# Optimization experiments

Measured on AMD Instinct MI355X. Metric: run time of the kernel, lower is better.

The kernel has to match this reference:

```python
import jax, jax.numpy as jnp
import numpy as np

B, T, N, E, H, L, K = 2, 32, 256, 1024, 16, 2, 256
MAXLEN = 512  # RelativeMultiheadAttention max_seq_len default
SCALES = (1, 2, 4)
TAU = 1.0


def setup_inputs() -> dict:
    key = jax.random.key(0)
    ks = jax.random.split(key, 9)
    s = 0.02
    A = 2 * L  # [layer0-spatial, layer0-temporal, layer1-spatial, layer1-temporal]
    return {
        "x": jax.random.normal(ks[0], (B, T, N, E), jnp.float32),
        "attn_wq": jax.random.normal(ks[1], (A, E, E), jnp.float32) * s,
        "attn_bq": jnp.zeros((A, E), jnp.float32),
        "attn_wk": jax.random.normal(ks[2], (A, E, E), jnp.float32) * s,
        "attn_bk": jnp.zeros((A, E), jnp.float32),
        "attn_wv": jax.random.normal(ks[3], (A, E, E), jnp.float32) * s,
        "attn_bv": jnp.zeros((A, E), jnp.float32),
        "attn_wd": jax.random.normal(ks[4], (A, E, E), jnp.float32) * s,
        "attn_bd": jnp.zeros((A, E), jnp.float32),
        "rel_bias": jax.random.normal(ks[5], (A, 2 * MAXLEN - 1, H), jnp.float32) * s,
        "sel_w": jax.random.normal(ks[6], (E, K), jnp.float32) * s,
        "sel_b": jnp.zeros((K,), jnp.float32),
    }


def _rel_attn(x, wq, bq, wk, bk, wv, bv, wd, bd, rb):
    # x: [Bx, S, E]; rb: [2*MAXLEN-1, H]
    Bx, S, _ = x.shape
    D = E // H
    q = (x @ wq + bq).reshape(Bx, S, H, D)
    k = (x @ wk + bk).reshape(Bx, S, H, D)
    v = (x @ wv + bv).reshape(Bx, S, H, D)
    scores = jnp.einsum('bshd,bthd->bhst', q, k) / jnp.sqrt(jnp.asarray(D, x.dtype))
    pos = jnp.arange(S)
    idx = pos[None, :] - pos[:, None] + (MAXLEN - 1)  # [S, S]
    bias = rb[idx]  # [S, S, H] gathered relative-position bias
    scores = scores + bias.transpose(2, 0, 1)[None]
    w = jax.nn.softmax(scores, axis=-1)
    ctx = jnp.einsum('bhst,bthd->bshd', w, v).reshape(Bx, S, E)
    return ctx @ wd + bd


def reference(x, attn_wq, attn_bq, attn_wk, attn_bk, attn_wv, attn_bv,
              attn_wd, attn_bd, rel_bias, sel_w, sel_b):
    h = x
    for l in range(L):
        # spatial attention over tokens within each frame
        i = 2 * l
        hs = h.reshape(B * T, N, E)
        hs = _rel_attn(hs, attn_wq[i], attn_bq[i], attn_wk[i], attn_bk[i],
                       attn_wv[i], attn_bv[i], attn_wd[i], attn_bd[i], rel_bias[i])
        # temporal attention across frames per spatial location
        j = 2 * l + 1
        ht = hs.reshape(B, T, N, E).transpose(0, 2, 1, 3).reshape(B * N, T, E)
        ht = _rel_attn(ht, attn_wq[j], attn_bq[j], attn_wk[j], attn_bk[j],
                       attn_wv[j], attn_bv[j], attn_wd[j], attn_bd[j], rel_bias[j])
        h = ht.reshape(B, N, T, E).transpose(0, 2, 1, 3)
    # DifferentiableTokenSelection: softmax-weighted pooling into K tokens
    flat = h.reshape(B, T * N, E)
    sc = flat @ sel_w + sel_b  # [B, T*N, K]
    wts = jax.nn.softmax(sc / TAU, axis=1)
    sel = jnp.einsum('bmk,bme->bke', wts, flat)  # [B, K, E]
    # multi-scale average pooling (kernel==stride==scale), concat along tokens
    outs = [sel.reshape(B, K // s, s, E).mean(axis=2) for s in SCALES]
    return jnp.concatenate(outs, axis=1)  # [B, K + K//2 + K//4, E]
```

## Files before the change

### kernel.cpp

```cpp
#include <hip/hip_runtime.h>
#include <stdint.h>


using f16x8 = __attribute__((ext_vector_type(8))) _Float16;
using f16x4 = __attribute__((ext_vector_type(4))) _Float16;
using f32x4 = __attribute__((ext_vector_type(4))) float;

__device__ __forceinline__ int tmap_dev(int m) {
    int bx = m >> 5;
    int s  = m & 31;
    int b  = bx >> 8;
    int n  = bx & 255;
    return (((b << 5) + s) << 8) + n;
}

__device__ __forceinline__ void load16(const _Float16* g, _Float16* l)
{
    __builtin_amdgcn_global_load_lds(
        (const __attribute__((address_space(1))) unsigned int*)g,
        (__attribute__((address_space(3))) unsigned int*)l,
        16, 0, 0);
}

__device__ __forceinline__ void split_f16(float v, _Float16& h, _Float16& l)
{
    h = (_Float16)v;
    l = (_Float16)(v - (float)h);
}

__global__ __launch_bounds__(256)
void conv_act(const float* __restrict__ src, _Float16* __restrict__ dh,
              _Float16* __restrict__ dl, int m_off)
{
    int idx = blockIdx.x * 256 + threadIdx.x;
    int e = idx << 3;
    int ml = e >> 10, col = e & 1023;
    const float* s = src + (size_t)(m_off + ml) * 1024 + col;
    float4 a = *(const float4*)s;
    float4 b = *(const float4*)(s + 4);
    float vv[8] = {a.x, a.y, a.z, a.w, b.x, b.y, b.z, b.w};
    f16x8 vh, vl;
    #pragma unroll
    for (int r = 0; r < 8; r++) {
        _Float16 h, l;
        split_f16(vv[r], h, l);
        vh[r] = h; vl[r] = l;
    }
    *(f16x8*)(dh + (size_t)ml * 1024 + col) = vh;
    *(f16x8*)(dl + (size_t)ml * 1024 + col) = vl;
}

__global__ __launch_bounds__(256)
void conv_wT(const float* __restrict__ W, _Float16* __restrict__ Th,
             _Float16* __restrict__ Tl, int ncols)
{
    __shared__ float Ls[64][65];
    const int n0 = blockIdx.x * 64, k0 = blockIdx.y * 64;
    const int t = threadIdx.x;
    const int kk = t >> 4, nn = (t & 15) << 2;
    #pragma unroll
    for (int i = 0; i < 4; i++) {
        float4 v = *(const float4*)(W + (size_t)(k0 + kk + 16 * i) * ncols + n0 + nn);
        Ls[kk + 16 * i][nn + 0] = v.x; Ls[kk + 16 * i][nn + 1] = v.y;
        Ls[kk + 16 * i][nn + 2] = v.z; Ls[kk + 16 * i][nn + 3] = v.w;
    }
    __syncthreads();
    const int nl = t >> 4, kc = (t & 15) << 2;
    #pragma unroll
    for (int i = 0; i < 4; i++) {
        int n = nl + 16 * i;
        f16x4 hh, ll;
        #pragma unroll
        for (int c = 0; c < 4; c++) {
            _Float16 h, l;
            split_f16(Ls[kc + c][n], h, l);
            hh[c] = h; ll[c] = l;
        }
        *(f16x4*)(Th + (size_t)(n0 + n) * 1024 + k0 + kc) = hh;
        *(f16x4*)(Tl + (size_t)(n0 + n) * 1024 + k0 + kc) = ll;
    }
}

template<int EPI>
__device__ __forceinline__ void gemm_core(
    const _Float16* __restrict__ Ah, const _Float16* __restrict__ Al,
    const _Float16* __restrict__ Wh, const _Float16* __restrict__ Wl,
    const float* __restrict__ bias,
    float* __restrict__ C, _Float16* __restrict__ Ch, _Float16* __restrict__ Cl,
    int ldc, int map_in, int m_off_in, int map_out, int m_off_out,
    int n0, int m0)
{
    __shared__ uint32_t smem_u[8512];
    _Float16* smem = (_Float16*)smem_u;
    _Float16* sAh = smem;
    _Float16* sAl = smem + 4096;
    _Float16* sBh = smem + 8192;
    _Float16* sBl = smem + 12288;

    const int tid = threadIdx.x;
    const int lane = tid & 63;
    const int wv = tid >> 6;
    const int fm = (wv >> 1) << 6;
    const int fn = (wv & 1) << 6;
    const int lm = lane & 15, lq = lane >> 4;

    f32x4 acc[4][4] = {};

    const int srow = tid >> 2;
    const int skc  = (tid & 3) << 3;
    const int gm0 = m_off_in + m0 + srow;
    const int gm1 = gm0 + 64;
    const int r0 = map_in ? tmap_dev(gm0) : gm0;
    const int r1 = map_in ? tmap_dev(gm1) : gm1;
    const _Float16* gAh0 = Ah + (size_t)r0 * 1024 + skc;
    const _Float16* gAh1 = Ah + (size_t)r1 * 1024 + skc;
    const _Float16* gAl0 = Al + (size_t)r0 * 1024 + skc;
    const _Float16* gAl1 = Al + (size_t)r1 * 1024 + skc;
    const _Float16* gB0 = Wh + (size_t)(n0 + srow) * 1024 + skc;
    const _Float16* gB1 = Wl + (size_t)(n0 + srow) * 1024 + skc;
    const int lo = tid << 3;

    for (int k0 = 0; k0 < 1024; k0 += 32) {
        load16(gAh0 + k0, sAh + lo);
        load16(gAh1 + k0, sAh + lo + 2048);
        load16(gAl0 + k0, sAl + lo);
        load16(gAl1 + k0, sAl + lo + 2048);
        load16(gB0 + k0,         sBh + lo);
        load16(gB0 + k0 + 65536, sBh + lo + 2048);
        load16(gB1 + k0,         sBl + lo);
        load16(gB1 + k0 + 65536, sBl + lo + 2048);
        __syncthreads();

        f16x8 ah[4], al[4], bh[4], bl[4];
        #pragma unroll
        for (int i = 0; i < 4; i++) {
            int ra = (fm + i * 16 + lm) * 32 + lq * 8;
            ah[i] = *(const f16x8*)(sAh + ra);
            al[i] = *(const f16x8*)(sAl + ra);
            int rb_ = (fn + i * 16 + lm) * 32 + lq * 8;
            bh[i] = *(const f16x8*)(sBh + rb_);
            bl[i] = *(const f16x8*)(sBl + rb_);
        }
        #pragma unroll
        for (int i = 0; i < 4; i++)
            #pragma unroll
            for (int j = 0; j < 4; j++) {
                acc[i][j] = __builtin_amdgcn_mfma_f32_16x16x32_f16(ah[i], bh[j], acc[i][j], 0, 0, 0);
                acc[i][j] = __builtin_amdgcn_mfma_f32_16x16x32_f16(ah[i], bl[j], acc[i][j], 0, 0, 0);
                acc[i][j] = __builtin_amdgcn_mfma_f32_16x16x32_f16(al[i], bh[j], acc[i][j], 0, 0, 0);
            }
        __syncthreads();
    }

    if (EPI == 0 || EPI == 1) {
        #pragma unroll
        for (int j = 0; j < 4; j++) {
            int n = n0 + fn + j * 16 + lm;
            float bb = bias[n];
            #pragma unroll
            for (int i = 0; i < 4; i++) {
                #pragma unroll
                for (int r = 0; r < 4; r++) {
                    int gm = m_off_out + m0 + fm + i * 16 + lq * 4 + r;
                    int row = map_out ? tmap_dev(gm) : gm;
                    float v = acc[i][j][r] + bb;
                    if (EPI == 0) {
                        C[(size_t)row * ldc + n] = v;
                    } else {
                        _Float16 h, l;
                        split_f16(v, h, l);
                        Ch[(size_t)row * 1024 + n] = h;
                        Cl[(size_t)row * 1024 + n] = l;
                    }
                }
            }
        }
    } else {
        const int fmh = fm >> 6;
        #pragma unroll
        for (int mh = 0; mh < 2; mh++) {
            __syncthreads();
            if (fmh == mh) {
                #pragma unroll
                for (int j = 0; j < 4; j++) {
                    int n = fn + j * 16 + lm;
                    float bb = bias[n0 + n];
                    #pragma unroll
                    for (int i = 0; i < 4; i++) {
                        #pragma unroll
                        for (int r = 0; r < 4; r++) {
                            float v = acc[i][j][r] + bb;
                            _Float16 h, l;
                            split_f16(v, h, l);
                            uint32_t ph = (uint32_t)__builtin_bit_cast(unsigned short, h);
                            uint32_t pl = (uint32_t)__builtin_bit_cast(unsigned short, l);
                            smem_u[(i * 16 + lq * 4 + r) * 133 + n] = ph | (pl << 16);
                        }
                    }
                }
            }
            __syncthreads();
            #pragma unroll
            for (int g = 0; g < 8; g++) {
                int u = tid + g * 256;
                int nn = u >> 4;
                int mg = (u & 15) << 2;
                uint32_t p0 = smem_u[(mg + 0) * 133 + nn];
                uint32_t p1 = smem_u[(mg + 1) * 133 + nn];
                uint32_t p2 = smem_u[(mg + 2) * 133 + nn];
                uint32_t p3 = smem_u[(mg + 3) * 133 + nn];
                f16x4 hh, ll;
                hh[0] = __builtin_bit_cast(_Float16, (unsigned short)(p0 & 0xffff));
                hh[1] = __builtin_bit_cast(_Float16, (unsigned short)(p1 & 0xffff));
                hh[2] = __builtin_bit_cast(_Float16, (unsigned short)(p2 & 0xffff));
                hh[3] = __builtin_bit_cast(_Float16, (unsigned short)(p3 & 0xffff));
                ll[0] = __builtin_bit_cast(_Float16, (unsigned short)(p0 >> 16));
                ll[1] = __builtin_bit_cast(_Float16, (unsigned short)(p1 >> 16));
                ll[2] = __builtin_bit_cast(_Float16, (unsigned short)(p2 >> 16));
                ll[3] = __builtin_bit_cast(_Float16, (unsigned short)(p3 >> 16));
                size_t off = (size_t)(n0 + nn) * 8192 + (m0 + mh * 64 + mg);
                *(f16x4*)(Ch + off) = hh;
                *(f16x4*)(Cl + off) = ll;
            }
        }
    }
}

__global__ __launch_bounds__(256, 2)
void gemm_f16s_f32(const _Float16* __restrict__ Ah, const _Float16* __restrict__ Al,
                   int map_in, int m_off_in,
                   const _Float16* __restrict__ Wh, const _Float16* __restrict__ Wl,
                   const float* __restrict__ bias, float* __restrict__ C, int ldc,
                   int map_out, int m_off_out)
{
    gemm_core<0>(Ah, Al, Wh, Wl, bias, C, nullptr, nullptr, ldc,
                 map_in, m_off_in, map_out, m_off_out,
                 blockIdx.x * 128, blockIdx.y * 128);
}

template<int EPI>
__device__ __forceinline__ void gemm256_core(
    uint32_t* __restrict__ smem_u,
    const _Float16* __restrict__ Ah, const _Float16* __restrict__ Al,
    const _Float16* __restrict__ Wh, const _Float16* __restrict__ Wl,
    const float* __restrict__ bias,
    _Float16* __restrict__ Ch, _Float16* __restrict__ Cl,
    int map_in, int m_off_in, int map_out, int m_off_out,
    int n0, int m0)
{
    _Float16* S = (_Float16*)smem_u;
    const int tid  = threadIdx.x;
    const int lane = tid & 63;
    const int wv = tid >> 6;
    const int wm = wv >> 1;
    const int fm = wm << 6;
    const int fn = (wv & 1) << 6;
    const int lm = lane & 15, lq = lane >> 4;
    const int ko = ((lq ^ ((lm >> 1) & 3)) << 3);

    f32x4 acc[4][4] = {};

    const int srow = tid >> 2;
    const int scol = (((tid & 3) ^ ((tid >> 3) & 3)) << 3);
    const int gm0 = m_off_in + m0 + srow;
    const int gm1 = gm0 + 128;
    const int r0 = map_in ? tmap_dev(gm0) : gm0;
    const int r1 = map_in ? tmap_dev(gm1) : gm1;
    const _Float16* gAh0 = Ah + (size_t)r0 * 1024 + scol;
    const _Float16* gAh1 = Ah + (size_t)r1 * 1024 + scol;
    const _Float16* gAl0 = Al + (size_t)r0 * 1024 + scol;
    const _Float16* gAl1 = Al + (size_t)r1 * 1024 + scol;
    const _Float16* gBh  = Wh + (size_t)(n0 + srow) * 1024 + scol;
    const _Float16* gBl  = Wl + (size_t)(n0 + srow) * 1024 + scol;
    const int lo = tid << 3;

    auto stage = [&](int t, int b) {
        const int k0 = t << 5;
        _Float16* d = S + b * 24576;
        load16(gAh0 + k0, d + lo);
        load16(gAh1 + k0, d + 4096  + lo);
        load16(gAl0 + k0, d + 8192  + lo);
        load16(gAl1 + k0, d + 12288 + lo);
        load16(gBh  + k0, d + 16384 + lo);
        load16(gBl  + k0, d + 20480 + lo);
    };

    auto kstep = [&](int t, int cb, int sb, bool last) {
        if (last) asm volatile("s_waitcnt vmcnt(0) lgkmcnt(0)" ::: "memory");
        else      asm volatile("s_waitcnt vmcnt(6) lgkmcnt(0)" ::: "memory");
        __builtin_amdgcn_s_barrier();
        if (sb >= 0) stage(t + 2, sb);

        const _Float16* c = S + cb * 24576;
        f16x8 ah[4], al[4], bh[4], bl[4];
        #pragma unroll
        for (int i = 0; i < 4; i++) {
            int ra = (fm + i * 16 + lm) * 32 + ko;
            ah[i] = *(const f16x8*)(c + ra);
            al[i] = *(const f16x8*)(c + 8192 + ra);
            int rb = (fn + i * 16 + lm) * 32 + ko;
            bh[i] = *(const f16x8*)(c + 16384 + rb);
            bl[i] = *(const f16x8*)(c + 20480 + rb);
        }
        __builtin_amdgcn_s_setprio(1);
        #pragma unroll
        for (int i = 0; i < 4; i++)
            #pragma unroll
            for (int j = 0; j < 4; j++) {
                acc[i][j] = __builtin_amdgcn_mfma_f32_16x16x32_f16(ah[i], bh[j], acc[i][j], 0, 0, 0);
                acc[i][j] = __builtin_amdgcn_mfma_f32_16x16x32_f16(ah[i], bl[j], acc[i][j], 0, 0, 0);
                acc[i][j] = __builtin_amdgcn_mfma_f32_16x16x32_f16(al[i], bh[j], acc[i][j], 0, 0, 0);
            }
        __builtin_amdgcn_s_setprio(0);
    };

    stage(0, 0);
    stage(1, 1);
    #pragma unroll 1
    for (int tt = 0; tt < 30; tt += 3) {
        kstep(tt + 0, 0, 2, false);
        kstep(tt + 1, 1, 0, false);
        kstep(tt + 2, 2, 1, false);
    }
    kstep(30, 0, -1, false);
    kstep(31, 1, -1, true);

    if (EPI == 1) {
        #pragma unroll
        for (int j = 0; j < 4; j++) {
            int n = n0 + fn + j * 16 + lm;
            float bb = bias[n];
            #pragma unroll
            for (int i = 0; i < 4; i++) {
                #pragma unroll
                for (int r = 0; r < 4; r++) {
                    int gm = m_off_out + m0 + fm + i * 16 + lq * 4 + r;
                    int row = map_out ? tmap_dev(gm) : gm;
                    float v = acc[i][j][r] + bb;
                    _Float16 h, l;
                    split_f16(v, h, l);
                    Ch[(size_t)row * 1024 + n] = h;
                    Cl[(size_t)row * 1024 + n] = l;
                }
            }
        }
    } else {
        #pragma unroll 1
        for (int q = 0; q < 4; q++) {
            __syncthreads();
            if (wm == q) {
                #pragma unroll
                for (int j = 0; j < 4; j++) {
                    int ncol = fn + j * 16 + lm;
                    float bb = bias[n0 + ncol];
                    #pragma unroll
                    for (int i = 0; i < 4; i++) {
                        #pragma unroll
                        for (int r = 0; r < 4; r++) {
                            float v = acc[i][j][r] + bb;
                            _Float16 h, l;
                            split_f16(v, h, l);
                            uint32_t ph = (uint32_t)__builtin_bit_cast(unsigned short, h);
                            uint32_t pl = (uint32_t)__builtin_bit_cast(unsigned short, l);
                            smem_u[(i * 16 + lq * 4 + r) * 129 + ncol] = ph | (pl << 16);
                        }
                    }
                }
            }
            __syncthreads();
            #pragma unroll
            for (int g = 0; g < 4; g++) {
                int u = tid + g * 512;
                int nn = u >> 4;
                int mg = (u & 15) << 2;
                uint32_t p0 = smem_u[(mg + 0) * 129 + nn];
                uint32_t p1 = smem_u[(mg + 1) * 129 + nn];
                uint32_t p2 = smem_u[(mg + 2) * 129 + nn];
                uint32_t p3 = smem_u[(mg + 3) * 129 + nn];
                f16x4 hh, ll;
                hh[0] = __builtin_bit_cast(_Float16, (unsigned short)(p0 & 0xffff));
                hh[1] = __builtin_bit_cast(_Float16, (unsigned short)(p1 & 0xffff));
                hh[2] = __builtin_bit_cast(_Float16, (unsigned short)(p2 & 0xffff));
                hh[3] = __builtin_bit_cast(_Float16, (unsigned short)(p3 & 0xffff));
                ll[0] = __builtin_bit_cast(_Float16, (unsigned short)(p0 >> 16));
                ll[1] = __builtin_bit_cast(_Float16, (unsigned short)(p1 >> 16));
                ll[2] = __builtin_bit_cast(_Float16, (unsigned short)(p2 >> 16));
                ll[3] = __builtin_bit_cast(_Float16, (unsigned short)(p3 >> 16));
                size_t off = (size_t)(n0 + nn) * 8192 + (m0 + q * 64 + mg);
                *(f16x4*)(Ch + off) = hh;
                *(f16x4*)(Cl + off) = ll;
            }
        }
    }
}

__global__ __launch_bounds__(512, 2)
void gemm_qkv256(const _Float16* __restrict__ Ah, const _Float16* __restrict__ Al,
                 int map_in, int m_off_in,
                 const _Float16* __restrict__ WTh, const _Float16* __restrict__ WTl,
                 const float* __restrict__ bq, const float* __restrict__ bk,
                 const float* __restrict__ bv,
                 _Float16* __restrict__ Qh, _Float16* __restrict__ Ql,
                 _Float16* __restrict__ Kh, _Float16* __restrict__ Kl,
                 _Float16* __restrict__ VTh, _Float16* __restrict__ VTl)
{
    __shared__ uint32_t smem_u[36864];
    const int bid = blockIdx.x;
    const int wg = (bid & 7) * 96 + (bid >> 3);
    const int z = wg >> 8;
    const int rem = wg & 255;
    const int m0 = (rem >> 3) << 8;
    const int n0 = (rem & 7) << 7;
    const _Float16* wh = WTh + (size_t)z * 1048576;
    const _Float16* wl = WTl + (size_t)z * 1048576;
    if (z < 2) {
        const float* bb = (z == 0) ? bq : bk;
        _Float16* oh = (z == 0) ? Qh : Kh;
        _Float16* ol = (z == 0) ? Ql : Kl;
        gemm256_core<1>(smem_u, Ah, Al, wh, wl, bb, oh, ol,
                        map_in, m_off_in, 0, 0, n0, m0);
    } else {
        gemm256_core<3>(smem_u, Ah, Al, wh, wl, bv, VTh, VTl,
                        map_in, m_off_in, 0, 0, n0, m0);
    }
}

__global__ __launch_bounds__(512, 2)
void gemm_h256(const _Float16* __restrict__ Ah, const _Float16* __restrict__ Al,
               int map_in, int m_off_in,
               const _Float16* __restrict__ Wh, const _Float16* __restrict__ Wl,
               const float* __restrict__ bias,
               _Float16* __restrict__ Ch, _Float16* __restrict__ Cl,
               int map_out, int m_off_out)
{
    __shared__ uint32_t smem_u[36864];
    const int bid = blockIdx.x;
    const int wg = (bid & 7) * 32 + (bid >> 3);
    const int m0 = (wg >> 3) << 8;
    const int n0 = (wg & 7) << 7;
    gemm256_core<1>(smem_u, Ah, Al, Wh, Wl, bias, Ch, Cl,
                    map_in, m_off_in, map_out, m_off_out, n0, m0);
}

__global__ __launch_bounds__(256, 2)
void attn_s_m(const _Float16* __restrict__ Qh, const _Float16* __restrict__ Ql,
              const _Float16* __restrict__ Kh, const _Float16* __restrict__ Kl,
              const _Float16* __restrict__ VTh, const _Float16* __restrict__ VTl,
              const float* __restrict__ RB,
              _Float16* __restrict__ Ch, _Float16* __restrict__ Cl)
{
    __shared__ _Float16 sKh[2048], sKl[2048];
    __shared__ _Float16 sVh[2560], sVl[2560];
    __shared__ _Float16 sPh[4][2560], sPl[4][2560];
    __shared__ float Bt[512];

    const int tid = threadIdx.x;
    const int lane = tid & 63;
    const int w = tid >> 6;
    const int lm = lane & 15, lq = lane >> 4;
    const int frame = blockIdx.x;
    const int h = blockIdx.y;
    const int rowbase = frame * 256;

    #pragma unroll
    for (int l = 0; l < 2; l++) {
        int idx = tid + l * 256;
        if (idx < 511) Bt[idx] = RB[(size_t)(256 + idx) * 16 + h];
    }

    f16x8 qbh[4][2], qbl[4][2];
    #pragma unroll
    for (int st = 0; st < 4; st++)
        #pragma unroll
        for (int kk = 0; kk < 2; kk++) {
            size_t qo = (size_t)(rowbase + w * 64 + st * 16 + lm) * 1024
                        + h * 64 + kk * 32 + lq * 8;
            qbh[st][kk] = *(const f16x8*)(Qh + qo);
            qbl[st][kk] = *(const f16x8*)(Ql + qo);
        }

    f32x4 cacc[4][4] = {};
    float lsum[4] = {0.f, 0.f, 0.f, 0.f};
    _Float16* Ph = sPh[w];
    _Float16* Pl = sPl[w];

    const int skrow = tid >> 3, skd = (tid & 7) << 3;
    const int svrow = tid >> 2, svj = (tid & 3) << 3;

    for (int jc = 0; jc < 8; jc++) {
        __syncthreads();
        {
            size_t ko = (size_t)(rowbase + jc * 32 + skrow) * 1024 + h * 64 + skd;
            *(f16x8*)(sKh + skrow * 64 + skd) = *(const f16x8*)(Kh + ko);
            *(f16x8*)(sKl + skrow * 64 + skd) = *(const f16x8*)(Kl + ko);
            size_t vo = (size_t)(h * 64 + svrow) * 8192 + rowbase + jc * 32 + svj;
            *(f16x8*)(sVh + svrow * 40 + svj) = *(const f16x8*)(VTh + vo);
            *(f16x8*)(sVl + svrow * 40 + svj) = *(const f16x8*)(VTl + vo);
        }
        __syncthreads();

        f32x4 sacc[2][4] = {};
        #pragma unroll
        for (int jt = 0; jt < 2; jt++) {
            f16x8 kah[2], kal[2];
            #pragma unroll
            for (int kk = 0; kk < 2; kk++) {
                int ra = (jt * 16 + lm) * 64 + kk * 32 + lq * 8;
                kah[kk] = *(const f16x8*)(sKh + ra);
                kal[kk] = *(const f16x8*)(sKl + ra);
            }
            #pragma unroll
            for (int st = 0; st < 4; st++)
                #pragma unroll
                for (int kk = 0; kk < 2; kk++) {
                    sacc[jt][st] = __builtin_amdgcn_mfma_f32_16x16x32_f16(kah[kk], qbh[st][kk], sacc[jt][st], 0, 0, 0);
                    sacc[jt][st] = __builtin_amdgcn_mfma_f32_16x16x32_f16(kah[kk], qbl[st][kk], sacc[jt][st], 0, 0, 0);
                    sacc[jt][st] = __builtin_amdgcn_mfma_f32_16x16x32_f16(kal[kk], qbh[st][kk], sacc[jt][st], 0, 0, 0);
                }
        }

        #pragma unroll
        for (int jt = 0; jt < 2; jt++)
            #pragma unroll
            for (int st = 0; st < 4; st++) {
                f16x4 p4h, p4l;
                #pragma unroll
                for (int r = 0; r < 4; r++) {
                    int j = jc * 32 + jt * 16 + lq * 4 + r;
                    int s = w * 64 + st * 16 + lm;
                    float p = __expf(sacc[jt][st][r] * 0.125f + Bt[j - s + 255]);
                    lsum[st] += p;
                    _Float16 hp, lp;
                    split_f16(p, hp, lp);
                    p4h[r] = hp; p4l[r] = lp;
                }
                int pa = (st * 16 + lm) * 40 + jt * 16 + lq * 4;
                *(f16x4*)(Ph + pa) = p4h;
                *(f16x4*)(Pl + pa) = p4l;
            }

        #pragma unroll
        for (int st = 0; st < 4; st++) {
            int pb = (st * 16 + lm) * 40 + lq * 8;
            f16x8 pbh = *(const f16x8*)(Ph + pb);
            f16x8 pbl = *(const f16x8*)(Pl + pb);
            #pragma unroll
            for (int dt = 0; dt < 4; dt++) {
                int va = (dt * 16 + lm) * 40 + lq * 8;
                f16x8 vah = *(const f16x8*)(sVh + va);
                f16x8 val = *(const f16x8*)(sVl + va);
                cacc[dt][st] = __builtin_amdgcn_mfma_f32_16x16x32_f16(vah, pbh, cacc[dt][st], 0, 0, 0);
                cacc[dt][st] = __builtin_amdgcn_mfma_f32_16x16x32_f16(vah, pbl, cacc[dt][st], 0, 0, 0);
                cacc[dt][st] = __builtin_amdgcn_mfma_f32_16x16x32_f16(val, pbh, cacc[dt][st], 0, 0, 0);
            }
        }
    }

    float inv[4];
    #pragma unroll
    for (int st = 0; st < 4; st++) {
        float t = lsum[st];
        t += __shfl_xor(t, 16);
        t += __shfl_xor(t, 32);
        inv[st] = 1.0f / t;
    }

    #pragma unroll
    for (int st = 0; st < 4; st++)
        #pragma unroll
        for (int dt = 0; dt < 4; dt++) {
            f16x4 oh, ol;
            #pragma unroll
            for (int r = 0; r < 4; r++) {
                _Float16 hp, lp;
                split_f16(cacc[dt][st][r] * inv[st], hp, lp);
                oh[r] = hp; ol[r] = lp;
            }
            size_t oo = (size_t)(rowbase + w * 64 + st * 16 + lm) * 1024
                        + h * 64 + dt * 16 + lq * 4;
            *(f16x4*)(Ch + oo) = oh;
            *(f16x4*)(Cl + oo) = ol;
        }
}

__global__ __launch_bounds__(256, 2)
void attn_t_m(const _Float16* __restrict__ Qh, const _Float16* __restrict__ Ql,
              const _Float16* __restrict__ Kh, const _Float16* __restrict__ Kl,
              const _Float16* __restrict__ VTh, const _Float16* __restrict__ VTl,
              const float* __restrict__ RB,
              _Float16* __restrict__ Ch, _Float16* __restrict__ Cl)
{
    __shared__ _Float16 sPh[4][1280], sPl[4][1280];
    __shared__ float Bt[64];

    const int tid = threadIdx.x;
    const int lane = tid & 63;
    const int w = tid >> 6;
    const int lm = lane & 15, lq = lane >> 4;
    const int h = blockIdx.y;
    const int bx = blockIdx.x * 4 + w;
    const int rowbase = bx * 32;

    if (tid < 63) Bt[tid] = RB[(size_t)(480 + tid) * 16 + h];
    __syncthreads();

    f16x8 qbh[2][2], qbl[2][2];
    #pragma unroll
    for (int st = 0; st < 2; st++)
        #pragma unroll
        for (int kk = 0; kk < 2; kk++) {
            size_t qo = (size_t)(rowbase + st * 16 + lm) * 1024 + h * 64 + kk * 32 + lq * 8;
            qbh[st][kk] = *(const f16x8*)(Qh + qo);
            qbl[st][kk] = *(const f16x8*)(Ql + qo);
        }

    f32x4 sacc[2][2] = {};
    #pragma unroll
    for (int jt = 0; jt < 2; jt++) {
        f16x8 kah[2], kal[2];
        #pragma unroll
        for (int kk = 0; kk < 2; kk++) {
            size_t ko = (size_t)(rowbase + jt * 16 + lm) * 1024 + h * 64 + kk * 32 + lq * 8;
            kah[kk] = *(const f16x8*)(Kh + ko);
            kal[kk] = *(const f16x8*)(Kl + ko);
        }
        #pragma unroll
        for (int st = 0; st < 2; st++)
            #pragma unroll
            for (int kk = 0; kk < 2; kk++) {
                sacc[jt][st] = __builtin_amdgcn_mfma_f32_16x16x32_f16(kah[kk], qbh[st][kk], sacc[jt][st], 0, 0, 0);
                sacc[jt][st] = __builtin_amdgcn_mfma_f32_16x16x32_f16(kah[kk], qbl[st][kk], sacc[jt][st], 0, 0, 0);
                sacc[jt][st] = __builtin_amdgcn_mfma_f32_16x16x32_f16(kal[kk], qbh[st][kk], sacc[jt][st], 0, 0, 0);
            }
    }

    float lsum[2] = {0.f, 0.f};
    _Float16* Ph = sPh[w];
    _Float16* Pl = sPl[w];
    #pragma unroll
    for (int jt = 0; jt < 2; jt++)
        #pragma unroll
        for (int st = 0; st < 2; st++) {
            f16x4 p4h, p4l;
            #pragma unroll
            for (int r = 0; r < 4; r++) {
                int j = jt * 16 + lq * 4 + r;
                int s = st * 16 + lm;
                float p = __expf(sacc[jt][st][r] * 0.125f + Bt[j - s + 31]);
                lsum[st] += p;
                _Float16 hp, lp;
                split_f16(p, hp, lp);
                p4h[r] = hp; p4l[r] = lp;
            }
            int pa = (st * 16 + lm) * 40 + jt * 16 + lq * 4;
            *(f16x4*)(Ph + pa) = p4h;
            *(f16x4*)(Pl + pa) = p4l;
        }

    f16x8 vah[4], val[4];
    #pragma unroll
    for (int dt = 0; dt < 4; dt++) {
        size_t vo = (size_t)(h * 64 + dt * 16 + lm) * 8192 + rowbase + lq * 8;
        vah[dt] = *(const f16x8*)(VTh + vo);
        val[dt] = *(const f16x8*)(VTl + vo);
    }
    f32x4 cacc[4][2] = {};
    #pragma unroll
    for (int st = 0; st < 2; st++) {
        int pb = (st * 16 + lm) * 40 + lq * 8;
        f16x8 pbh = *(const f16x8*)(Ph + pb);
        f16x8 pbl = *(const f16x8*)(Pl + pb);
        #pragma unroll
        for (int dt = 0; dt < 4; dt++) {
            cacc[dt][st] = __builtin_amdgcn_mfma_f32_16x16x32_f16(vah[dt], pbh, cacc[dt][st], 0, 0, 0);
            cacc[dt][st] = __builtin_amdgcn_mfma_f32_16x16x32_f16(vah[dt], pbl, cacc[dt][st], 0, 0, 0);
            cacc[dt][st] = __builtin_amdgcn_mfma_f32_16x16x32_f16(val[dt], pbh, cacc[dt][st], 0, 0, 0);
        }
    }

    float inv[2];
    #pragma unroll
    for (int st = 0; st < 2; st++) {
        float t = lsum[st];
        t += __shfl_xor(t, 16);
        t += __shfl_xor(t, 32);
        inv[st] = 1.0f / t;
    }

    #pragma unroll
    for (int st = 0; st < 2; st++)
        #pragma unroll
        for (int dt = 0; dt < 4; dt++) {
            f16x4 oh, ol;
            #pragma unroll
            for (int r = 0; r < 4; r++) {
                _Float16 hp, lp;
                split_f16(cacc[dt][st][r] * inv[st], hp, lp);
                oh[r] = hp; ol[r] = lp;
            }
            size_t oo = (size_t)(rowbase + st * 16 + lm) * 1024 + h * 64 + dt * 16 + lq * 4;
            *(f16x4*)(Ch + oo) = oh;
            *(f16x4*)(Cl + oo) = ol;
        }
}

__global__ __launch_bounds__(256)
void colsum_part_kernel(const float* __restrict__ SC, float* __restrict__ P)
{
    int bid = blockIdx.x;
    int b = bid >> 7, chunk = bid & 127;
    int base = b * 8192 + chunk * 64;
    int k = threadIdx.x;
    float sum = 0.0f;
    for (int r = 0; r < 64; r++)
        sum += __expf(SC[(size_t)(base + r) * 256 + k]);
    P[(size_t)bid * 256 + k] = sum;
}

__global__ __launch_bounds__(256)
void colsum_reduce_kernel(const float* __restrict__ P, float* __restrict__ CS)
{
    int b = blockIdx.x;
    int k = threadIdx.x;
    float s = 0.0f;
    for (int c = 0; c < 128; c++)
        s += P[(size_t)(b * 128 + c) * 256 + k];
    CS[b * 256 + k] = s;
}

__global__ __launch_bounds__(256)
void trans_wts(const float* __restrict__ SC, const float* __restrict__ CS,
               _Float16* __restrict__ Th, _Float16* __restrict__ Tl)
{
    __shared__ float L[64][65];
    const int mt = blockIdx.x * 64;
    const int kt = blockIdx.y * 64;
    const int b  = mt >> 13;
    const int ml = mt & 8191;
    const int tid = threadIdx.x;
    #pragma unroll
    for (int l = 0; l < 4; l++) {
        int idx = tid + 256 * l;
        int r = idx >> 4, c4 = (idx & 15) << 2;
        float4 v = *(const float4*)(SC + (size_t)(mt + r) * 256 + kt + c4);
        L[r][c4 + 0] = __expf(v.x); L[r][c4 + 1] = __expf(v.y);
        L[r][c4 + 2] = __expf(v.z); L[r][c4 + 3] = __expf(v.w);
    }
    __syncthreads();
    #pragma unroll
    for (int l = 0; l < 4; l++) {
        int idx = tid + 256 * l;
        int rk = idx >> 4, c4 = (idx & 15) << 2;
        float inv = 1.0f / CS[b * 256 + kt + rk];
        f16x4 hh, ll;
        #pragma unroll
        for (int u = 0; u < 4; u++) {
            _Float16 h, l2;
            split_f16(L[c4 + u][rk] * inv, h, l2);
            hh[u] = h; ll[u] = l2;
        }
        size_t o = ((size_t)b * 256 + kt + rk) * 8192 + ml + c4;
        *(f16x4*)(Th + o) = hh;
        *(f16x4*)(Tl + o) = ll;
    }
}

__global__ __launch_bounds__(256)
void trans_f16(const _Float16* __restrict__ Sh, const _Float16* __restrict__ Sl,
               _Float16* __restrict__ Th, _Float16* __restrict__ Tl)
{
    __shared__ _Float16 L[64][72];
    const int mt = blockIdx.x * 64, et = blockIdx.y * 64;
    const _Float16* S = blockIdx.z ? Sl : Sh;
    _Float16* T = blockIdx.z ? Tl : Th;
    const int tid = threadIdx.x;
    #pragma unroll
    for (int l = 0; l < 2; l++) {
        int v = tid * 2 + l;
        int r = v >> 3, c8 = (v & 7) << 3;
        *(f16x8*)&L[r][c8] = *(const f16x8*)(S + (size_t)(mt + r) * 1024 + et + c8);
    }
    __syncthreads();
    #pragma unroll
    for (int l = 0; l < 2; l++) {
        int v = tid * 2 + l;
        int r = v >> 3, c8 = (v & 7) << 3;
        f16x8 o;
        #pragma unroll
        for (int u = 0; u < 8; u++) o[u] = L[c8 + u][r];
        *(f16x8*)(T + (size_t)(et + r) * 16384 + mt + c8) = o;
    }
}

__global__ __launch_bounds__(256, 2)
void gemm_selm(const _Float16* __restrict__ Wth, const _Float16* __restrict__ Wtl,
               const _Float16* __restrict__ Hth, const _Float16* __restrict__ Htl,
               float* __restrict__ P)
{
    __shared__ _Float16 sAh[4096], sAl[4096], sBh[4096], sBl[4096];
    const int tid = threadIdx.x;
    const int lane = tid & 63;
    const int wv = tid >> 6;
    const int fm = (wv >> 1) << 6;
    const int fn = (wv & 1) << 6;
    const int lm = lane & 15, lq = lane >> 4;
    const int n0 = blockIdx.x * 128;
    const int m0 = blockIdx.y * 128;
    const int z  = blockIdx.z;
    const int b = z >> 3, sp = z & 7;

    f32x4 acc[4][4] = {};

    const int srow = tid >> 2;
    const int skc  = (tid & 3) << 3;
    const _Float16* gAh0 = Wth + ((size_t)b * 256 + m0 + srow) * 8192 + sp * 1024 + skc;
    const _Float16* gAl0 = Wtl + ((size_t)b * 256 + m0 + srow) * 8192 + sp * 1024 + skc;
    const _Float16* gB0 = Hth + (size_t)(n0 + srow) * 16384 + b * 8192 + sp * 1024 + skc;
    const _Float16* gB1 = Htl + (size_t)(n0 + srow) * 16384 + b * 8192 + sp * 1024 + skc;
    const int lo = tid << 3;

    for (int k0 = 0; k0 < 1024; k0 += 32) {
        load16(gAh0 + k0,          sAh + lo);
        load16(gAh0 + k0 + 524288, sAh + lo + 2048);
        load16(gAl0 + k0,          sAl + lo);
        load16(gAl0 + k0 + 524288, sAl + lo + 2048);
        load16(gB0 + k0,           sBh + lo);
        load16(gB0 + k0 + 1048576, sBh + lo + 2048);
        load16(gB1 + k0,           sBl + lo);
        load16(gB1 + k0 + 1048576, sBl + lo + 2048);
        __syncthreads();

        f16x8 ah[4], al[4], bh[4], bl[4];
        #pragma unroll
        for (int i = 0; i < 4; i++) {
            int ra = (fm + i * 16 + lm) * 32 + lq * 8;
            ah[i] = *(const f16x8*)(sAh + ra);
            al[i] = *(const f16x8*)(sAl + ra);
            int rb_ = (fn + i * 16 + lm) * 32 + lq * 8;
            bh[i] = *(const f16x8*)(sBh + rb_);
            bl[i] = *(const f16x8*)(sBl + rb_);
        }
        #pragma unroll
        for (int i = 0; i < 4; i++)
            #pragma unroll
            for (int j = 0; j < 4; j++) {
                acc[i][j] = __builtin_amdgcn_mfma_f32_16x16x32_f16(ah[i], bh[j], acc[i][j], 0, 0, 0);
                acc[i][j] = __builtin_amdgcn_mfma_f32_16x16x32_f16(ah[i], bl[j], acc[i][j], 0, 0, 0);
                acc[i][j] = __builtin_amdgcn_mfma_f32_16x16x32_f16(al[i], bh[j], acc[i][j], 0, 0, 0);
            }
        __syncthreads();
    }

    float* Pz = P + (size_t)z * 262144;
    #pragma unroll
    for (int j = 0; j < 4; j++) {
        int n = n0 + fn + j * 16 + lm;
        #pragma unroll
        for (int i = 0; i < 4; i++)
            #pragma unroll
            for (int r = 0; r < 4; r++) {
                int k = m0 + fm + i * 16 + lq * 4 + r;
                Pz[(size_t)k * 1024 + n] = acc[i][j][r];
            }
    }
}

__global__ __launch_bounds__(256)
void sel_reduce(const float* __restrict__ P, float* __restrict__ SEL)
{
    int idx4 = blockIdx.x * 256 + threadIdx.x;
    int e = idx4 << 2;
    int b = e >> 18;
    int rest = e & 262143;
    const float* p = P + (size_t)(b * 8) * 262144 + rest;
    float4 acc = {0.f, 0.f, 0.f, 0.f};
    #pragma unroll
    for (int s = 0; s < 8; s++) {
        float4 v = *(const float4*)(p + (size_t)s * 262144);
        acc.x += v.x; acc.y += v.y; acc.z += v.z; acc.w += v.w;
    }
    *(float4*)(SEL + e) = acc;
}

__global__ __launch_bounds__(256)
void pool_kernel(const float* __restrict__ SEL, float* __restrict__ out)
{
    int i4 = blockIdx.x * 256 + threadIdx.x;
    int e  = i4 << 2;
    int row = e >> 10;
    int b = row / 448;
    int r = row - b * 448;
    int c = e & 1023;
    const float* sb = SEL + (size_t)b * (256 * 1024);
    float4 o;
    if (r < 256) {
        o = *(const float4*)(sb + (size_t)r * 1024 + c);
    } else if (r < 384) {
        int r2 = (r - 256) * 2;
        float4 x0 = *(const float4*)(sb + (size_t)r2 * 1024 + c);
        float4 x1 = *(const float4*)(sb + (size_t)(r2 + 1) * 1024 + c);
        o.x = 0.5f * (x0.x + x1.x); o.y = 0.5f * (x0.y + x1.y);
        o.z = 0.5f * (x0.z + x1.z); o.w = 0.5f * (x0.w + x1.w);
    } else {
        int r4 = (r - 384) * 4;
        float4 x0 = *(const float4*)(sb + (size_t)(r4 + 0) * 1024 + c);
        float4 x1 = *(const float4*)(sb + (size_t)(r4 + 1) * 1024 + c);
        float4 x2 = *(const float4*)(sb + (size_t)(r4 + 2) * 1024 + c);
        float4 x3 = *(const float4*)(sb + (size_t)(r4 + 3) * 1024 + c);
        o.x = 0.25f * (x0.x + x1.x + x2.x + x3.x);
        o.y = 0.25f * (x0.y + x1.y + x2.y + x3.y);
        o.z = 0.25f * (x0.z + x1.z + x2.z + x3.z);
        o.w = 0.25f * (x0.w + x1.w + x2.w + x3.w);
    }
    *(float4*)(out + e) = o;
}

extern "C" void kernel_launch(void* const* d_in, const int* in_sizes, int n_in,
                              void* d_out, int out_size, void* d_ws, size_t ws_size,
                              hipStream_t stream)
{
    const float* x    = (const float*)d_in[0];
    const float* wq   = (const float*)d_in[1];
    const float* bq   = (const float*)d_in[2];
    const float* wk   = (const float*)d_in[3];
    const float* bk   = (const float*)d_in[4];
    const float* wv   = (const float*)d_in[5];
    const float* bv   = (const float*)d_in[6];
    const float* wd   = (const float*)d_in[7];
    const float* bd   = (const float*)d_in[8];
    const float* rb   = (const float*)d_in[9];
    const float* selw = (const float*)d_in[10];
    const float* selb = (const float*)d_in[11];
    float* out = (float*)d_out;

    float* base = (float*)d_ws;
    _Float16* Hh  = (_Float16*)base;
    _Float16* Hl  = Hh + 16777216;
    _Float16* Qh  = (_Float16*)(base + 16777216);
    _Float16* Ql  = Qh + 8388608;
    _Float16* Kh  = Ql + 8388608;
    _Float16* Kl  = Kh + 8388608;
    _Float16* VTh = (_Float16*)(base + 33554432);
    _Float16* VTl = VTh + 8388608;
    _Float16* CXh = (_Float16*)(base + 41943040);
    _Float16* CXl = CXh + 8388608;
    _Float16* WTh = (_Float16*)(base + 50331648);
    _Float16* WTl = WTh + 4194304;
    _Float16* Ah  = (_Float16*)(base + 54525952);
    _Float16* Al  = Ah + 8388608;
    float* SC   = (float*)Qh;
    float* Pp   = (float*)Kh;
    float* SEL  = (float*)Kl;
    float* PART = SEL + 524288;
    float* CSUM = PART + 65536;
    _Float16* WTTh = CXh;
    _Float16* WTTl = CXl;
    _Float16* HTh  = Ah;
    _Float16* HTl  = VTh;

    const dim3 blk(256);
    const dim3 blk2(512);

    for (int a = 0; a < 4; a++) {
        const int mi = (a & 1);
        const size_t wo = (size_t)a * 1048576;
        const int bo = a * 1024;
        const float* rba = rb + (size_t)a * 1023 * 16;

        conv_wT<<<dim3(16, 16), blk, 0, stream>>>(wq + wo, WTh,           WTl,           1024);
        conv_wT<<<dim3(16, 16), blk, 0, stream>>>(wk + wo, WTh + 1048576, WTl + 1048576, 1024);
        conv_wT<<<dim3(16, 16), blk, 0, stream>>>(wv + wo, WTh + 2097152, WTl + 2097152, 1024);
        conv_wT<<<dim3(16, 16), blk, 0, stream>>>(wd + wo, WTh + 3145728, WTl + 3145728, 1024);

        for (int c = 0; c < 2; c++) {
            const int mo = c * 8192;
            const _Float16 *sH, *sL;
            int sm, so;
            if (a == 0) {
                conv_act<<<4096, blk, 0, stream>>>(x, Ah, Al, mo);
                sH = Ah; sL = Al; sm = 0; so = 0;
            } else {
                sH = Hh; sL = Hl; sm = mi; so = mo;
            }
            gemm_qkv256<<<dim3(768), blk2, 0, stream>>>(
                sH, sL, sm, so, WTh, WTl, bq + bo, bk + bo, bv + bo,
                Qh, Ql, Kh, Kl, VTh, VTl);
            if (mi == 0)
                attn_s_m<<<dim3(32, 16), blk, 0, stream>>>(Qh, Ql, Kh, Kl, VTh, VTl, rba, CXh, CXl);
            else
                attn_t_m<<<dim3(64, 16), blk, 0, stream>>>(Qh, Ql, Kh, Kl, VTh, VTl, rba, CXh, CXl);
            gemm_h256<<<dim3(256), blk2, 0, stream>>>(
                CXh, CXl, 0, 0, WTh + 3145728, WTl + 3145728, bd + bo, Hh, Hl, mi, mo);
        }
    }

    conv_wT<<<dim3(4, 16), blk, 0, stream>>>(selw, WTh, WTl, 256);
    gemm_f16s_f32<<<dim3(2, 128), blk, 0, stream>>>(
        Hh, Hl, 0, 0, WTh, WTl, selb, SC, 256, 0, 0);
    colsum_part_kernel<<<256, blk, 0, stream>>>(SC, PART);
    colsum_reduce_kernel<<<2, blk, 0, stream>>>(PART, CSUM);
    trans_wts<<<dim3(256, 4), blk, 0, stream>>>(SC, CSUM, WTTh, WTTl);
    trans_f16<<<dim3(256, 16, 2), blk, 0, stream>>>(Hh, Hl, HTh, HTl);
    gemm_selm<<<dim3(8, 2, 16), blk, 0, stream>>>(WTTh, WTTl, HTh, HTl, Pp);
    sel_reduce<<<512, blk, 0, stream>>>(Pp, SEL);
    pool_kernel<<<896, blk, 0, stream>>>(SEL, out);
}
```

Before: 2.124 ms.

## Interleave GEMM mainloop into barrier-separated phases and stage EPI1 stores via LDS

Splits each k-step of the 256-row GEMM into four phases, one per B column fragment. Each phase issues a part of the next tile's global-to-LDS loads, then runs MFMAs between explicit barriers and sched_barriers, aiming at a finer interleave of memory and matrix work across waves. The EPI==1 epilogue for this kernel now goes through LDS and writes 16-byte vector stores of the hi/lo halves instead of scattered 2-byte stores. The dead EPI1/EPI2 paths in the older gemm_core are removed. The extra barriers per k-step add synchronisation cost and could hurt if waves stall.

```diff
diff --git a/kernel.cpp b/kernel.cpp
--- a/kernel.cpp
+++ b/kernel.cpp
@@ -152,7 +152,7 @@
         __syncthreads();
     }
 
-    if (EPI == 0 || EPI == 1) {
+    if (EPI == 0) {
         #pragma unroll
         for (int j = 0; j < 4; j++) {
             int n = n0 + fn + j * 16 + lm;
@@ -163,64 +163,8 @@
                 for (int r = 0; r < 4; r++) {
                     int gm = m_off_out + m0 + fm + i * 16 + lq * 4 + r;
                     int row = map_out ? tmap_dev(gm) : gm;
-                    float v = acc[i][j][r] + bb;
-                    if (EPI == 0) {
-                        C[(size_t)row * ldc + n] = v;
-                    } else {
-                        _Float16 h, l;
-                        split_f16(v, h, l);
-                        Ch[(size_t)row * 1024 + n] = h;
-                        Cl[(size_t)row * 1024 + n] = l;
-                    }
+                    C[(size_t)row * ldc + n] = acc[i][j][r] + bb;
                 }
-            }
-        }
-    } else {
-        const int fmh = fm >> 6;
-        #pragma unroll
-        for (int mh = 0; mh < 2; mh++) {
-            __syncthreads();
-            if (fmh == mh) {
-                #pragma unroll
-                for (int j = 0; j < 4; j++) {
-                    int n = fn + j * 16 + lm;
-                    float bb = bias[n0 + n];
-                    #pragma unroll
-                    for (int i = 0; i < 4; i++) {
-                        #pragma unroll
-                        for (int r = 0; r < 4; r++) {
-                            float v = acc[i][j][r] + bb;
-                            _Float16 h, l;
-                            split_f16(v, h, l);
-                            uint32_t ph = (uint32_t)__builtin_bit_cast(unsigned short, h);
-                            uint32_t pl = (uint32_t)__builtin_bit_cast(unsigned short, l);
-                            smem_u[(i * 16 + lq * 4 + r) * 133 + n] = ph | (pl << 16);
-                        }
-                    }
-                }
-            }
-            __syncthreads();
-            #pragma unroll
-            for (int g = 0; g < 8; g++) {
-                int u = tid + g * 256;
-                int nn = u >> 4;
-                int mg = (u & 15) << 2;
-                uint32_t p0 = smem_u[(mg + 0) * 133 + nn];
-                uint32_t p1 = smem_u[(mg + 1) * 133 + nn];
-                uint32_t p2 = smem_u[(mg + 2) * 133 + nn];
-                uint32_t p3 = smem_u[(mg + 3) * 133 + nn];
-                f16x4 hh, ll;
-                hh[0] = __builtin_bit_cast(_Float16, (unsigned short)(p0 & 0xffff));
-                hh[1] = __builtin_bit_cast(_Float16, (unsigned short)(p1 & 0xffff));
-                hh[2] = __builtin_bit_cast(_Float16, (unsigned short)(p2 & 0xffff));
-                hh[3] = __builtin_bit_cast(_Float16, (unsigned short)(p3 & 0xffff));
-                ll[0] = __builtin_bit_cast(_Float16, (unsigned short)(p0 >> 16));
-                ll[1] = __builtin_bit_cast(_Float16, (unsigned short)(p1 >> 16));
-                ll[2] = __builtin_bit_cast(_Float16, (unsigned short)(p2 >> 16));
-                ll[3] = __builtin_bit_cast(_Float16, (unsigned short)(p3 >> 16));
-                size_t off = (size_t)(n0 + nn) * 8192 + (m0 + mh * 64 + mg);
-                *(f16x4*)(Ch + off) = hh;
-                *(f16x4*)(Cl + off) = ll;
             }
         }
     }
@@ -274,74 +218,134 @@
     const _Float16* gBl  = Wl + (size_t)(n0 + srow) * 1024 + scol;
     const int lo = tid << 3;
 
-    auto stage = [&](int t, int b) {
+    auto stage_part = [&](int t, int b, int part) {
         const int k0 = t << 5;
         _Float16* d = S + b * 24576;
-        load16(gAh0 + k0, d + lo);
-        load16(gAh1 + k0, d + 4096  + lo);
-        load16(gAl0 + k0, d + 8192  + lo);
-        load16(gAl1 + k0, d + 12288 + lo);
-        load16(gBh  + k0, d + 16384 + lo);
-        load16(gBl  + k0, d + 20480 + lo);
+        if (part == 0) {
+            load16(gAh0 + k0, d + lo);
+            load16(gAh1 + k0, d + 4096  + lo);
+        } else if (part == 1) {
+            load16(gAl0 + k0, d + 8192  + lo);
+            load16(gAl1 + k0, d + 12288 + lo);
+        } else {
+            load16(gBh  + k0, d + 16384 + lo);
+            load16(gBl  + k0, d + 20480 + lo);
+        }
     };
 
-    auto kstep = [&](int t, int cb, int sb, bool last) {
-        if (last) asm volatile("s_waitcnt vmcnt(0) lgkmcnt(0)" ::: "memory");
-        else      asm volatile("s_waitcnt vmcnt(6) lgkmcnt(0)" ::: "memory");
-        __builtin_amdgcn_s_barrier();
-        if (sb >= 0) stage(t + 2, sb);
-
+    auto kstep = [&](int t, int cb, int sb, int vmN) {
         const _Float16* c = S + cb * 24576;
-        f16x8 ah[4], al[4], bh[4], bl[4];
+        f16x8 ah[4], al[4];
+
         #pragma unroll
         for (int i = 0; i < 4; i++) {
             int ra = (fm + i * 16 + lm) * 32 + ko;
             ah[i] = *(const f16x8*)(c + ra);
             al[i] = *(const f16x8*)(c + 8192 + ra);
-            int rb = (fn + i * 16 + lm) * 32 + ko;
-            bh[i] = *(const f16x8*)(c + 16384 + rb);
-            bl[i] = *(const f16x8*)(c + 20480 + rb);
-        }
-        __builtin_amdgcn_s_setprio(1);
-        #pragma unroll
-        for (int i = 0; i < 4; i++)
-            #pragma unroll
-            for (int j = 0; j < 4; j++) {
-                acc[i][j] = __builtin_amdgcn_mfma_f32_16x16x32_f16(ah[i], bh[j], acc[i][j], 0, 0, 0);
-                acc[i][j] = __builtin_amdgcn_mfma_f32_16x16x32_f16(ah[i], bl[j], acc[i][j], 0, 0, 0);
-                acc[i][j] = __builtin_amdgcn_mfma_f32_16x16x32_f16(al[i], bh[j], acc[i][j], 0, 0, 0);
-            }
-        __builtin_amdgcn_s_setprio(0);
+        }
+        {
+            int rb = (fn + lm) * 32 + ko;
+            f16x8 bh = *(const f16x8*)(c + 16384 + rb);
+            f16x8 bl = *(const f16x8*)(c + 20480 + rb);
+            if (sb >= 0) stage_part(t + 2, sb, 0);
+            __builtin_amdgcn_s_barrier();
+            asm volatile("s_waitcnt lgkmcnt(0)" ::: "memory");
+            __builtin_amdgcn_sched_barrier(0);
+            __builtin_amdgcn_s_setprio(1);
+            #pragma unroll
+            for (int i = 0; i < 4; i++) {
+                acc[i][0] = __builtin_amdgcn_mfma_f32_16x16x32_f16(ah[i], bh, acc[i][0], 0, 0, 0);
+                acc[i][0] = __builtin_amdgcn_mfma_f32_16x16x32_f16(ah[i], bl, acc[i][0], 0, 0, 0);
+                acc[i][0] = __builtin_amdgcn_mfma_f32_16x16x32_f16(al[i], bh, acc[i][0], 0, 0, 0);
+            }
+            __builtin_amdgcn_s_setprio(0);
+            __builtin_amdgcn_s_barrier();
+        }
+
+        #pragma unroll
+        for (int j = 1; j < 4; j++) {
+            int rb = (fn + j * 16 + lm) * 32 + ko;
+            f16x8 bh = *(const f16x8*)(c + 16384 + rb);
+            f16x8 bl = *(const f16x8*)(c + 20480 + rb);
+            if (j < 3) {
+                if (sb >= 0) stage_part(t + 2, sb, j);
+            } else {
+                if (vmN == 6)      asm volatile("s_waitcnt vmcnt(6)" ::: "memory");
+                else if (vmN == 0) asm volatile("s_waitcnt vmcnt(0)" ::: "memory");
+            }
+            __builtin_amdgcn_s_barrier();
+            asm volatile("s_waitcnt lgkmcnt(0)" ::: "memory");
+            __builtin_amdgcn_sched_barrier(0);
+            __builtin_amdgcn_s_setprio(1);
+            #pragma unroll
+            for (int i = 0; i < 4; i++) {
+                acc[i][j] = __builtin_amdgcn_mfma_f32_16x16x32_f16(ah[i], bh, acc[i][j], 0, 0, 0);
+                acc[i][j] = __builtin_amdgcn_mfma_f32_16x16x32_f16(ah[i], bl, acc[i][j], 0, 0, 0);
+                acc[i][j] = __builtin_amdgcn_mfma_f32_16x16x32_f16(al[i], bh, acc[i][j], 0, 0, 0);
+            }
+            __builtin_amdgcn_s_setprio(0);
+            __builtin_amdgcn_s_barrier();
+        }
     };
 
-    stage(0, 0);
-    stage(1, 1);
+    #pragma unroll
+    for (int p = 0; p < 3; p++) stage_part(0, 0, p);
+    #pragma unroll
+    for (int p = 0; p < 3; p++) stage_part(1, 1, p);
+    asm volatile("s_waitcnt vmcnt(6)" ::: "memory");
+    __builtin_amdgcn_s_barrier();
+
     #pragma unroll 1
     for (int tt = 0; tt < 30; tt += 3) {
-        kstep(tt + 0, 0, 2, false);
-        kstep(tt + 1, 1, 0, false);
-        kstep(tt + 2, 2, 1, false);
-    }
-    kstep(30, 0, -1, false);
-    kstep(31, 1, -1, true);
+        kstep(tt + 0, 0, 2, 6);
+        kstep(tt + 1, 1, 0, 6);
+        kstep(tt + 2, 2, 1, 6);
+    }
+    kstep(30, 0, -1, 0);
+    kstep(31, 1, -1, -1);
 
     if (EPI == 1) {
-        #pragma unroll
-        for (int j = 0; j < 4; j++) {
-            int n = n0 + fn + j * 16 + lm;
-            float bb = bias[n];
-            #pragma unroll
-            for (int i = 0; i < 4; i++) {
+        #pragma unroll 1
+        for (int q = 0; q < 4; q++) {
+            __syncthreads();
+            if (wm == q) {
                 #pragma unroll
-                for (int r = 0; r < 4; r++) {
-                    int gm = m_off_out + m0 + fm + i * 16 + lq * 4 + r;
-                    int row = map_out ? tmap_dev(gm) : gm;
-                    float v = acc[i][j][r] + bb;
-                    _Float16 h, l;
-                    split_f16(v, h, l);
-                    Ch[(size_t)row * 1024 + n] = h;
-                    Cl[(size_t)row * 1024 + n] = l;
+                for (int j = 0; j < 4; j++) {
+                    int ncol = fn + j * 16 + lm;
+                    float bb = bias[n0 + ncol];
+                    #pragma unroll
+                    for (int i = 0; i < 4; i++) {
+                        #pragma unroll
+                        for (int r = 0; r < 4; r++) {
+                            float v = acc[i][j][r] + bb;
+                            _Float16 h, l;
+                            split_f16(v, h, l);
+                            uint32_t ph = (uint32_t)__builtin_bit_cast(unsigned short, h);
+                            uint32_t pl = (uint32_t)__builtin_bit_cast(unsigned short, l);
+                            smem_u[(i * 16 + lq * 4 + r) * 132 + ncol] = ph | (pl << 16);
+                        }
+                    }
                 }
+            }
+            __syncthreads();
+            #pragma unroll
+            for (int g = 0; g < 2; g++) {
+                int u = tid + g * 512;
+                int rl = u >> 4;
+                int c8 = (u & 15) << 3;
+                uint32_t p[8];
+                #pragma unroll
+                for (int x = 0; x < 8; x++) p[x] = smem_u[rl * 132 + c8 + x];
+                f16x8 hh, ll;
+                #pragma unroll
+                for (int x = 0; x < 8; x++) {
+                    hh[x] = __builtin_bit_cast(_Float16, (unsigned short)(p[x] & 0xffff));
+                    ll[x] = __builtin_bit_cast(_Float16, (unsigned short)(p[x] >> 16));
+                }
+                int gm = m_off_out + m0 + q * 64 + rl;
+                int row = map_out ? tmap_dev(gm) : gm;
+                *(f16x8*)(Ch + (size_t)row * 1024 + n0 + c8) = hh;
+                *(f16x8*)(Cl + (size_t)row * 1024 + n0 + c8) = ll;
             }
         }
     } else {
```

Result: slower. 2.184 ms (+2.8%).
